# Kernel optimization log

Measured on AMD Instinct MI355X. Metric: run time of the kernel, lower is better.

The kernel has to match this reference:

```python
import jax, jax.numpy as jnp
import numpy as np

CHUNK = 128
TAU = 0.7


def setup_inputs() -> dict:
    key = jax.random.key(0)
    ks = jax.random.split(key, 8)
    B, S, D, H, E = 4, 4096, 2048, 1024, 8
    x = jax.random.normal(ks[0], (B, S, D), dtype=jnp.float32)
    prev_expert_indices = jax.random.randint(ks[1], (B,), 0, E)
    # router MLP params (stored as [in, out]); xavier-uniform-like init, zero biases
    def xavier(k, fin, fout):
        lim = np.sqrt(6.0 / (fin + fout)).astype(np.float32)
        return jax.random.uniform(k, (fin, fout), jnp.float32, -lim, lim)
    w1 = xavier(ks[2], D, H)
    b1 = jnp.zeros((H,), jnp.float32)
    w2 = xavier(ks[3], H, H // 2)
    b2 = jnp.zeros((H // 2,), jnp.float32)
    w3 = jax.random.normal(ks[4], (H // 2, E), jnp.float32) * 0.02  # final layer std=0.02
    b3 = jnp.zeros((E,), jnp.float32)
    return {"x": x, "prev_expert_indices": prev_expert_indices,
            "w1": w1, "b1": b1, "w2": w2, "b2": b2, "w3": w3, "b3": b3}


def reference(x, prev_expert_indices, w1, b1, w2, b2, w3, b3):
    B, S, D = x.shape
    E = w3.shape[1]
    C = S // CHUNK  # num_chunks (seq_len divisible by chunk_size)

    # Router MLP on every token (Dropout is identity in eval), then per-chunk mean
    h = jax.nn.relu(x @ w1 + b1)
    h = jax.nn.relu(h @ w2 + b2)
    tok_logits = h @ w3 + b3                                   # [B, S, E]
    chunk_logits = tok_logits.reshape(B, C, CHUNK, E).mean(2)  # [B, C, E]

    top = jnp.argmax(chunk_logits, axis=-1).astype(jnp.int32)  # [B, C]

    # Sequential hysteresis over chunks (prev_expert_indices given => hysteresis active)
    def step(prev, inp):
        logits_c, top_c, is_first = inp  # [B,E], [B], scalar bool
        cur = jnp.take_along_axis(logits_c, top_c[:, None], axis=1)[:, 0]
        pv = jnp.take_along_axis(logits_c, prev[:, None], axis=1)[:, 0]
        switch = (cur - pv) > TAU
        final = jnp.where(is_first, top_c, jnp.where(switch, top_c, prev))
        flips = jnp.where(is_first, 0, switch.sum().astype(jnp.int32))
        return final, (final, flips)

    is_first = jnp.arange(C) == 0
    _, (experts_t, flips_t) = jax.lax.scan(
        step, jnp.zeros((B,), jnp.int32),
        (chunk_logits.transpose(1, 0, 2), top.T, is_first))
    expert_indices = experts_t.T                               # [B, C]

    one_hot = jax.nn.one_hot(expert_indices, E, dtype=jnp.float32)  # [B, C, E]
    routing_weights = jnp.broadcast_to(one_hot[:, :, None, :],
                                       (B, C, CHUNK, E)).reshape(B, S, E)

    # Stats
    probs = jax.nn.softmax(chunk_logits, axis=-1)
    gate_entropy = -(probs * jnp.log(probs + 1e-8)).sum(-1).mean()
    expert_utilization = one_hot.mean((0, 1))                  # [E]
    flip_rate = flips_t.sum().astype(jnp.float32) / (B * max(1, C - 1))
    routing_concentration = jnp.linalg.norm(expert_utilization)

    return (routing_weights, expert_indices, chunk_logits,
            gate_entropy, expert_utilization, flip_rate, routing_concentration)
```

## Files before the change

kernel.cpp:

```cpp
#include <hip/hip_runtime.h>
#include <math.h>

typedef _Float16 half_t;
typedef __attribute__((ext_vector_type(4))) _Float16 half4v;
typedef __attribute__((ext_vector_type(8))) _Float16 half8v;
typedef __attribute__((ext_vector_type(4))) float floatx4;

constexpr int B_ = 4, S_ = 4096, D_ = 2048, H_ = 1024, H2_ = 512, E_ = 8;
constexpr int CHUNK_ = 128;
constexpr int C_ = S_ / CHUNK_;
constexpr int M_ = B_ * S_;
constexpr float TAU_ = 0.7f;
constexpr float WSCALE = 64.0f, OSCALE = 1.0f / 64.0f;

constexpr int OUT_RW = 0;
constexpr int OUT_EI = OUT_RW + B_ * S_ * E_;
constexpr int OUT_CL = OUT_EI + B_ * C_;
constexpr int OUT_GE = OUT_CL + B_ * C_ * E_;
constexpr int OUT_UT = OUT_GE + 1;
constexpr int OUT_FR = OUT_UT + E_;
constexpr int OUT_RC = OUT_FR + 1;

__global__ __launch_bounds__(256)
void prep_kernel(const float* __restrict__ x, const float* __restrict__ w1,
                 const float* __restrict__ w2,
                 half_t* __restrict__ xh, half_t* __restrict__ w1t,
                 half_t* __restrict__ w2th, half_t* __restrict__ w2tl,
                 float* __restrict__ cl_acc)
{
    __shared__ float tile[32][33];
    const int tx = threadIdx.x & 31;
    const int ty = threadIdx.x >> 5;
    const int bid = blockIdx.x;

    if (bid < 8192) {
        const int base = bid * 1024 + threadIdx.x;
#pragma unroll
        for (int p = 0; p < 4; ++p) {
            const int i = base + p * 256;
            const float4 v = ((const float4*)x)[i];
            half4v h;
            h.x = (half_t)v.x; h.y = (half_t)v.y; h.z = (half_t)v.z; h.w = (half_t)v.w;
            ((half4v*)xh)[i] = h;
        }
    } else if (bid < 10240) {
        const int b2 = bid - 8192;
        const int n0 = (b2 & 31) * 32;
        const int k0 = (b2 >> 5) * 32;
#pragma unroll
        for (int r = 0; r < 4; ++r)
            tile[ty + r * 8][tx] = w1[(size_t)(k0 + ty + r * 8) * H_ + n0 + tx];
        __syncthreads();
#pragma unroll
        for (int r = 0; r < 4; ++r)
            w1t[(size_t)(n0 + ty + r * 8) * D_ + k0 + tx] = (half_t)tile[tx][ty + r * 8];
    } else if (bid < 10752) {
        const int b2 = bid - 10240;
        const int n0 = (b2 & 15) * 32;
        const int k0 = (b2 >> 4) * 32;
#pragma unroll
        for (int r = 0; r < 4; ++r)
            tile[ty + r * 8][tx] = w2[(size_t)(k0 + ty + r * 8) * H2_ + n0 + tx];
        __syncthreads();
#pragma unroll
        for (int r = 0; r < 4; ++r) {
            const float v = tile[tx][ty + r * 8] * WSCALE;
            const half_t h = (half_t)v;
            const size_t off = (size_t)(n0 + ty + r * 8) * H_ + k0 + tx;
            w2th[off] = h;
            w2tl[off] = (half_t)(v - (float)h);
        }
    } else {
        for (int i = threadIdx.x; i < B_ * C_ * E_; i += 256) cl_acc[i] = 0.0f;
    }
}

__global__ __launch_bounds__(256, 3)
void gemm1_kernel(const half_t* __restrict__ Ah,
                  const half_t* __restrict__ BTh,
                  const float* __restrict__ bias, half_t* __restrict__ outh)
{
    constexpr int KD = D_, ND = H_, BK = 32;
    __shared__ __align__(16) half_t sA[128 * BK];
    __shared__ __align__(16) half_t sB[128 * BK];

    const int tid = threadIdx.x;
    const int lane = tid & 63;
    const int wave = tid >> 6;
    const int wm = (wave & 1) * 64;
    const int wn = (wave >> 1) * 64;
    const int rowBlk = blockIdx.x * 16 + (blockIdx.y >> 3);
    const int colBlk = blockIdx.y & 7;
    const long blockM = (long)rowBlk * 128;
    const long blockN = (long)colBlk * 128;

    floatx4 acc[4][4];
#pragma unroll
    for (int i = 0; i < 4; ++i)
#pragma unroll
        for (int j = 0; j < 4; ++j) acc[i][j] = (floatx4){0.f, 0.f, 0.f, 0.f};

    const int srow = tid >> 2;
    const int skoff = (tid & 3) * 8;
    const int ldsoff = srow * BK + skoff;
    const int fr = lane & 15;
    const int fq = (lane >> 4) * 8;

    for (int k0 = 0; k0 < KD; k0 += BK) {
        __syncthreads();
#pragma unroll
        for (int p = 0; p < 2; ++p) {
            const int row = srow + p * 64;
            const size_t aoff = (size_t)(blockM + row) * KD + k0 + skoff;
            const size_t boff = (size_t)(blockN + row) * KD + k0 + skoff;
            const int loff = ldsoff + p * 2048;
            __builtin_amdgcn_global_load_lds(
                (const __attribute__((address_space(1))) void*)(Ah + aoff),
                (__attribute__((address_space(3))) void*)(sA + loff), 16, 0, 0);
            __builtin_amdgcn_global_load_lds(
                (const __attribute__((address_space(1))) void*)(BTh + boff),
                (__attribute__((address_space(3))) void*)(sB + loff), 16, 0, 0);
        }
        __syncthreads();

        half8v fb[4];
#pragma unroll
        for (int t = 0; t < 4; ++t)
            fb[t] = *(const half8v*)(sB + (wn + t * 16 + fr) * BK + fq);
#pragma unroll
        for (int i = 0; i < 4; ++i) {
            const half8v fa = *(const half8v*)(sA + (wm + i * 16 + fr) * BK + fq);
#pragma unroll
            for (int j = 0; j < 4; ++j)
                acc[i][j] = __builtin_amdgcn_mfma_f32_16x16x32_f16(fa, fb[j], acc[i][j], 0, 0, 0);
        }
    }

    const int orow = (lane >> 4) * 4;
    const int ocol = lane & 15;
#pragma unroll
    for (int j = 0; j < 4; ++j) {
        const long gn = blockN + wn + j * 16 + ocol;
        const float bj = bias[gn];
#pragma unroll
        for (int i = 0; i < 4; ++i) {
#pragma unroll
            for (int r = 0; r < 4; ++r) {
                const float v = fmaxf(acc[i][j][r] + bj, 0.0f);
                const size_t off = (size_t)(blockM + wm + i * 16 + orow + r) * ND + gn;
                outh[off] = (half_t)v;
            }
        }
    }
}

__global__ __launch_bounds__(256, 3)
void gemm2_fused_kernel(const half_t* __restrict__ Ah,
                        const half_t* __restrict__ BTh, const half_t* __restrict__ BTl,
                        const float* __restrict__ bias, const float* __restrict__ w3,
                        float* __restrict__ cl_acc)
{
    constexpr int KD = H_, BK = 32;
    __shared__ __align__(16) half_t sAh[128 * BK];
    __shared__ __align__(16) half_t sBh[128 * BK];
    __shared__ __align__(16) half_t sBl[128 * BK];

    const int tid = threadIdx.x;
    const int lane = tid & 63;
    const int wave = tid >> 6;
    const int wm = (wave & 1) * 64;
    const int wn = (wave >> 1) * 64;
    const int d = blockIdx.y * 4 + blockIdx.x;
    const int xcd = d & 7;
    const int l = d >> 3;
    const int rowBlk = xcd * 16 + (l >> 2);
    const int colBlk = l & 3;
    const long blockM = (long)rowBlk * 128;
    const long blockN = (long)colBlk * 128;

    floatx4 acc[4][4];
#pragma unroll
    for (int i = 0; i < 4; ++i)
#pragma unroll
        for (int j = 0; j < 4; ++j) acc[i][j] = (floatx4){0.f, 0.f, 0.f, 0.f};

    const int srow = tid >> 2;
    const int skoff = (tid & 3) * 8;
    const int ldsoff = srow * BK + skoff;
    const int fr = lane & 15;
    const int fq = (lane >> 4) * 8;

    for (int k0 = 0; k0 < KD; k0 += BK) {
        __syncthreads();
#pragma unroll
        for (int p = 0; p < 2; ++p) {
            const int row = srow + p * 64;
            const size_t aoff = (size_t)(blockM + row) * KD + k0 + skoff;
            const size_t boff = (size_t)(blockN + row) * KD + k0 + skoff;
            const int loff = ldsoff + p * 2048;
            __builtin_amdgcn_global_load_lds(
                (const __attribute__((address_space(1))) void*)(Ah + aoff),
                (__attribute__((address_space(3))) void*)(sAh + loff), 16, 0, 0);
            __builtin_amdgcn_global_load_lds(
                (const __attribute__((address_space(1))) void*)(BTh + boff),
                (__attribute__((address_space(3))) void*)(sBh + loff), 16, 0, 0);
            __builtin_amdgcn_global_load_lds(
                (const __attribute__((address_space(1))) void*)(BTl + boff),
                (__attribute__((address_space(3))) void*)(sBl + loff), 16, 0, 0);
        }
        __syncthreads();

        half8v fbh[4], fbl[4];
#pragma unroll
        for (int t = 0; t < 4; ++t) {
            fbh[t] = *(const half8v*)(sBh + (wn + t * 16 + fr) * BK + fq);
            fbl[t] = *(const half8v*)(sBl + (wn + t * 16 + fr) * BK + fq);
        }
#pragma unroll
        for (int i = 0; i < 4; ++i) {
            const half8v fah = *(const half8v*)(sAh + (wm + i * 16 + fr) * BK + fq);
#pragma unroll
            for (int j = 0; j < 4; ++j) {
                acc[i][j] = __builtin_amdgcn_mfma_f32_16x16x32_f16(fah, fbh[j], acc[i][j], 0, 0, 0);
                acc[i][j] = __builtin_amdgcn_mfma_f32_16x16x32_f16(fah, fbl[j], acc[i][j], 0, 0, 0);
            }
        }
    }

    const int ocol = lane & 15;
    float p[E_];
#pragma unroll
    for (int e = 0; e < E_; ++e) p[e] = 0.0f;
#pragma unroll
    for (int j = 0; j < 4; ++j) {
        const int gn = (int)blockN + wn + j * 16 + ocol;
        const float bj = bias[gn];
        const float4 w3a = *(const float4*)(w3 + (size_t)gn * E_);
        const float4 w3b = *(const float4*)(w3 + (size_t)gn * E_ + 4);
        float colsum = 0.0f;
#pragma unroll
        for (int i = 0; i < 4; ++i)
#pragma unroll
            for (int r = 0; r < 4; ++r)
                colsum += fmaxf(acc[i][j][r] * OSCALE + bj, 0.0f);
        p[0] += colsum * w3a.x; p[1] += colsum * w3a.y;
        p[2] += colsum * w3a.z; p[3] += colsum * w3a.w;
        p[4] += colsum * w3b.x; p[5] += colsum * w3b.y;
        p[6] += colsum * w3b.z; p[7] += colsum * w3b.w;
    }
#pragma unroll
    for (int e = 0; e < E_; ++e)
#pragma unroll
        for (int off = 32; off > 0; off >>= 1)
            p[e] += __shfl_xor(p[e], off);
#pragma unroll
    for (int e = 0; e < E_; ++e)
        if (lane == e) atomicAdd(&cl_acc[rowBlk * E_ + e], p[e]);
}

__global__ __launch_bounds__(256)
void final_route_kernel(const float* __restrict__ cl_acc, const float* __restrict__ b3,
                        float* __restrict__ out)
{
    __shared__ float cl[B_ * C_][E_];
    __shared__ int tops[B_ * C_];
    __shared__ int finals[B_ * C_];
    __shared__ int flips[B_];
    __shared__ float ent[B_ * C_];

    const int tid = threadIdx.x;

    if (tid < B_ * C_) {
        int best = 0;
        float bvv = -1e30f;
#pragma unroll
        for (int e = 0; e < E_; ++e) {
            const float v = cl_acc[tid * E_ + e] * (1.0f / CHUNK_) + b3[e];
            cl[tid][e] = v;
            if (v > bvv) { bvv = v; best = e; }
        }
        tops[tid] = best;
    }
    __syncthreads();

    if (tid < B_) {
        const int b = tid;
        int prev = 0, fl = 0;
        for (int c = 0; c < C_; ++c) {
            const int t = tops[b * C_ + c];
            int fin;
            if (c == 0) {
                fin = t;
            } else {
                const float cur = cl[b * C_ + c][t];
                const float pv = cl[b * C_ + c][prev];
                const bool sw = (cur - pv) > TAU_;
                if (sw) fl++;
                fin = sw ? t : prev;
            }
            finals[b * C_ + c] = fin;
            prev = fin;
        }
        flips[b] = fl;
    }
    __syncthreads();

    {
        const int tok = blockIdx.x * 256 + tid;
        const int b = tok >> 12;
        const int c = (tok & (S_ - 1)) >> 7;
        const int e = finals[b * C_ + c];
        float4 v0 = make_float4(e == 0 ? 1.f : 0.f, e == 1 ? 1.f : 0.f,
                                e == 2 ? 1.f : 0.f, e == 3 ? 1.f : 0.f);
        float4 v1 = make_float4(e == 4 ? 1.f : 0.f, e == 5 ? 1.f : 0.f,
                                e == 6 ? 1.f : 0.f, e == 7 ? 1.f : 0.f);
        float4* dst = (float4*)(out + OUT_RW + (size_t)tok * E_);
        dst[0] = v0;
        dst[1] = v1;
    }

    if (blockIdx.x == 0) {
        if (tid < B_ * C_) {
            out[OUT_EI + tid] = (float)finals[tid];
#pragma unroll
            for (int e = 0; e < E_; ++e) out[OUT_CL + tid * E_ + e] = cl[tid][e];
            float m = cl[tid][0];
            for (int e = 1; e < E_; ++e) m = fmaxf(m, cl[tid][e]);
            float pr[E_], s = 0.0f;
            for (int e = 0; e < E_; ++e) { pr[e] = expf(cl[tid][e] - m); s += pr[e]; }
            const float inv = 1.0f / s;
            float h = 0.0f;
            for (int e = 0; e < E_; ++e) { const float pe = pr[e] * inv; h -= pe * logf(pe + 1e-8f); }
            ent[tid] = h;
        }
        __syncthreads();
        if (tid == 0) {
            float esum = 0.0f;
            for (int i = 0; i < B_ * C_; ++i) esum += ent[i];
            out[OUT_GE] = esum / (float)(B_ * C_);

            int cnt[E_];
            for (int e = 0; e < E_; ++e) cnt[e] = 0;
            for (int i = 0; i < B_ * C_; ++i) cnt[finals[i]]++;
            float n2 = 0.0f;
            for (int e = 0; e < E_; ++e) {
                const float u = (float)cnt[e] / (float)(B_ * C_);
                out[OUT_UT + e] = u;
                n2 += u * u;
            }
            const int totfl = flips[0] + flips[1] + flips[2] + flips[3];
            out[OUT_FR] = (float)totfl / (float)(B_ * (C_ - 1));
            out[OUT_RC] = sqrtf(n2);
        }
    }
}

extern "C" void kernel_launch(void* const* d_in, const int* in_sizes, int n_in,
                              void* d_out, int out_size, void* d_ws, size_t ws_size,
                              hipStream_t stream)
{
    const float* x  = (const float*)d_in[0];
    const float* w1 = (const float*)d_in[2];
    const float* b1 = (const float*)d_in[3];
    const float* w2 = (const float*)d_in[4];
    const float* b2 = (const float*)d_in[5];
    const float* w3 = (const float*)d_in[6];
    const float* b3 = (const float*)d_in[7];
    float* out = (float*)d_out;

    half_t* xh   = (half_t*)d_ws;
    half_t* w1t  = xh + (size_t)M_ * D_;
    half_t* h1h  = w1t + (size_t)H_ * D_;
    half_t* w2th = h1h + (size_t)M_ * H_;
    half_t* w2tl = w2th + (size_t)H2_ * H_;
    float*  cl_acc = (float*)(w2tl + (size_t)H2_ * H_);

    prep_kernel<<<dim3(10753), dim3(256), 0, stream>>>(x, w1, w2, xh, w1t, w2th, w2tl, cl_acc);
    gemm1_kernel<<<dim3(H_ / 128, M_ / 128), dim3(256), 0, stream>>>(xh, w1t, b1, h1h);
    gemm2_fused_kernel<<<dim3(H2_ / 128, M_ / 128), dim3(256), 0, stream>>>(
        h1h, w2th, w2tl, b2, w3, cl_acc);
    final_route_kernel<<<dim3(M_ / 256), dim3(256), 0, stream>>>(cl_acc, b3, out);
}
```

Measured before the change: 352.1 us.

## Rewrite gemm1 as 256x256 tile kernel with multi-buffered LDS pipeline

```diff
diff --git a/kernel.cpp b/kernel.cpp
--- a/kernel.cpp
+++ b/kernel.cpp
@@ -75,80 +75,139 @@
     }
 }
 
-__global__ __launch_bounds__(256, 3)
+__device__ __forceinline__ void stage_half_g1(const half_t* __restrict__ g,
+                                              half_t* l, int tid)
+{
+#pragma unroll
+    for (int r = 0; r < 2; ++r) {
+        const int row = r * 128 + (tid >> 2);
+        const int cbh = ((tid & 3) * 8) ^ ((row & 3) << 3);
+        __builtin_amdgcn_global_load_lds(
+            (const __attribute__((address_space(1))) void*)(g + (size_t)row * D_ + cbh),
+            (__attribute__((address_space(3))) void*)(l + (r * 512 + tid) * 8),
+            16, 0, 0);
+    }
+}
+
+__global__ __launch_bounds__(512, 2)
 void gemm1_kernel(const half_t* __restrict__ Ah,
                   const half_t* __restrict__ BTh,
                   const float* __restrict__ bias, half_t* __restrict__ outh)
 {
-    constexpr int KD = D_, ND = H_, BK = 32;
-    __shared__ __align__(16) half_t sA[128 * BK];
-    __shared__ __align__(16) half_t sB[128 * BK];
+    constexpr int KD = D_;
+    constexpr int ND = H_;
+    constexpr int NT = KD / 64;
+
+    __shared__ __align__(16) half_t sA[2][2][256 * 32];
+    __shared__ __align__(16) half_t sB[2][2][256 * 32];
 
     const int tid = threadIdx.x;
     const int lane = tid & 63;
     const int wave = tid >> 6;
-    const int wm = (wave & 1) * 64;
-    const int wn = (wave >> 1) * 64;
-    const int rowBlk = blockIdx.x * 16 + (blockIdx.y >> 3);
-    const int colBlk = blockIdx.y & 7;
-    const long blockM = (long)rowBlk * 128;
-    const long blockN = (long)colBlk * 128;
-
-    floatx4 acc[4][4];
-#pragma unroll
-    for (int i = 0; i < 4; ++i)
+    const int wRow = (wave >> 2) * 128;
+    const int wCol = (wave & 3) * 64;
+    const int fr = lane & 15;
+    const int fqx = ((lane >> 4) * 8) ^ ((fr & 3) << 3);
+
+    const int bid = blockIdx.x;
+    const long blockM = (long)((bid & 7) * 8 + (bid >> 5)) * 256;
+    const long blockN = (long)((bid >> 3) & 3) * 256;
+
+    const half_t* gA = Ah + (size_t)blockM * KD;
+    const half_t* gB = BTh + (size_t)blockN * KD;
+
+    floatx4 acc[8][4];
+#pragma unroll
+    for (int i = 0; i < 8; ++i)
 #pragma unroll
         for (int j = 0; j < 4; ++j) acc[i][j] = (floatx4){0.f, 0.f, 0.f, 0.f};
 
-    const int srow = tid >> 2;
-    const int skoff = (tid & 3) * 8;
-    const int ldsoff = srow * BK + skoff;
-    const int fr = lane & 15;
-    const int fq = (lane >> 4) * 8;
-
-    for (int k0 = 0; k0 < KD; k0 += BK) {
-        __syncthreads();
-#pragma unroll
-        for (int p = 0; p < 2; ++p) {
-            const int row = srow + p * 64;
-            const size_t aoff = (size_t)(blockM + row) * KD + k0 + skoff;
-            const size_t boff = (size_t)(blockN + row) * KD + k0 + skoff;
-            const int loff = ldsoff + p * 2048;
-            __builtin_amdgcn_global_load_lds(
-                (const __attribute__((address_space(1))) void*)(Ah + aoff),
-                (__attribute__((address_space(3))) void*)(sA + loff), 16, 0, 0);
-            __builtin_amdgcn_global_load_lds(
-                (const __attribute__((address_space(1))) void*)(BTh + boff),
-                (__attribute__((address_space(3))) void*)(sB + loff), 16, 0, 0);
-        }
-        __syncthreads();
-
-        half8v fb[4];
-#pragma unroll
-        for (int t = 0; t < 4; ++t)
-            fb[t] = *(const half8v*)(sB + (wn + t * 16 + fr) * BK + fq);
-#pragma unroll
-        for (int i = 0; i < 4; ++i) {
-            const half8v fa = *(const half8v*)(sA + (wm + i * 16 + fr) * BK + fq);
-#pragma unroll
-            for (int j = 0; j < 4; ++j)
-                acc[i][j] = __builtin_amdgcn_mfma_f32_16x16x32_f16(fa, fb[j], acc[i][j], 0, 0, 0);
-        }
-    }
+    stage_half_g1(gA,      sA[0][0], tid);
+    stage_half_g1(gB,      sB[0][0], tid);
+    stage_half_g1(gA + 32, sA[0][1], tid);
+    stage_half_g1(gB + 32, sB[0][1], tid);
+    stage_half_g1(gB + 64, sB[1][0], tid);
+    stage_half_g1(gA + 64, sA[1][0], tid);
+    stage_half_g1(gB + 96, sB[1][1], tid);
+    asm volatile("s_waitcnt vmcnt(6)" ::: "memory");
+    __builtin_amdgcn_s_barrier();
+    __builtin_amdgcn_sched_barrier(0);
+
+    half8v bfr[4];
+
+#define G1_PHASE(BUF, H, MB, STAGE_STMT, TAIL_STMT)                            \
+    {                                                                          \
+        half8v afr[4];                                                         \
+        if ((MB) == 0) {                                                       \
+            _Pragma("unroll")                                                  \
+            for (int n = 0; n < 4; ++n)                                        \
+                bfr[n] = *(const half8v*)(sB[BUF][H] +                         \
+                          (wCol + n * 16 + fr) * 32 + fqx);                    \
+        }                                                                      \
+        _Pragma("unroll")                                                      \
+        for (int m = 0; m < 4; ++m)                                            \
+            afr[m] = *(const half8v*)(sA[BUF][H] +                             \
+                      (wRow + (MB) + m * 16 + fr) * 32 + fqx);                 \
+        STAGE_STMT;                                                            \
+        __builtin_amdgcn_s_barrier();                                          \
+        asm volatile("s_waitcnt lgkmcnt(0)" ::: "memory");                     \
+        __builtin_amdgcn_sched_barrier(0);                                     \
+        __builtin_amdgcn_s_setprio(1);                                         \
+        _Pragma("unroll")                                                      \
+        for (int m = 0; m < 4; ++m)                                            \
+            _Pragma("unroll")                                                  \
+            for (int n = 0; n < 4; ++n)                                        \
+                acc[(MB) / 16 + m][n] = __builtin_amdgcn_mfma_f32_16x16x32_f16(\
+                    afr[m], bfr[n], acc[(MB) / 16 + m][n], 0, 0, 0);           \
+        __builtin_amdgcn_s_setprio(0);                                         \
+        TAIL_STMT;                                                             \
+        __builtin_amdgcn_s_barrier();                                          \
+        __builtin_amdgcn_sched_barrier(0);                                     \
+    }
+
+#define G1_TILE(BUF, T)                                                        \
+    {                                                                          \
+        G1_PHASE(BUF, 0, 0,                                                    \
+            if ((T) + 1 < NT)                                                  \
+                stage_half_g1(gA + ((T) + 1) * 64 + 32, sA[(BUF) ^ 1][1], tid),\
+            );                                                                 \
+        G1_PHASE(BUF, 0, 64,                                                   \
+            if ((T) + 2 < NT)                                                  \
+                stage_half_g1(gB + ((T) + 2) * 64, sB[BUF][0], tid),           \
+            );                                                                 \
+        G1_PHASE(BUF, 1, 0,                                                    \
+            if ((T) + 2 < NT)                                                  \
+                stage_half_g1(gA + ((T) + 2) * 64, sA[BUF][0], tid),           \
+            );                                                                 \
+        G1_PHASE(BUF, 1, 64,                                                   \
+            if ((T) + 2 < NT)                                                  \
+                stage_half_g1(gB + ((T) + 2) * 64 + 32, sB[BUF][1], tid),      \
+            if ((T) < NT - 2) {                                                \
+                asm volatile("s_waitcnt vmcnt(6)" ::: "memory");               \
+            } else if ((T) == NT - 2) {                                        \
+                asm volatile("s_waitcnt vmcnt(0)" ::: "memory");               \
+            });                                                                \
+    }
+
+    for (int t = 0; t < NT; t += 2) {
+        G1_TILE(0, t);
+        G1_TILE(1, t + 1);
+    }
+#undef G1_TILE
+#undef G1_PHASE
 
     const int orow = (lane >> 4) * 4;
     const int ocol = lane & 15;
 #pragma unroll
-    for (int j = 0; j < 4; ++j) {
-        const long gn = blockN + wn + j * 16 + ocol;
+    for (int n = 0; n < 4; ++n) {
+        const long gn = blockN + wCol + n * 16 + ocol;
         const float bj = bias[gn];
 #pragma unroll
-        for (int i = 0; i < 4; ++i) {
+        for (int m = 0; m < 8; ++m) {
 #pragma unroll
             for (int r = 0; r < 4; ++r) {
-                const float v = fmaxf(acc[i][j][r] + bj, 0.0f);
-                const size_t off = (size_t)(blockM + wm + i * 16 + orow + r) * ND + gn;
-                outh[off] = (half_t)v;
+                const float v = fmaxf(acc[m][n][r] + bj, 0.0f);
+                outh[(size_t)(blockM + wRow + m * 16 + orow + r) * ND + gn] = (half_t)v;
             }
         }
     }
@@ -376,7 +435,7 @@
     float*  cl_acc = (float*)(w2tl + (size_t)H2_ * H_);
 
     prep_kernel<<<dim3(10753), dim3(256), 0, stream>>>(x, w1, w2, xh, w1t, w2th, w2tl, cl_acc);
-    gemm1_kernel<<<dim3(H_ / 128, M_ / 128), dim3(256), 0, stream>>>(xh, w1t, b1, h1h);
+    gemm1_kernel<<<dim3(256), dim3(512), 0, stream>>>(xh, w1t, b1, h1h);
     gemm2_fused_kernel<<<dim3(H2_ / 128, M_ / 128), dim3(256), 0, stream>>>(
         h1h, w2th, w2tl, b2, w3, cl_acc);
     final_route_kernel<<<dim3(M_ / 256), dim3(256), 0, stream>>>(cl_acc, b3, out);
```

New measurement: 351.3 us. About the same (-0.2%).
